# Optimization experiments

Hardware: AMD Instinct MI355X
Metric: run time of the kernel (lower is better)

The kernel has to match this reference:

```python
import jax, jax.numpy as jnp
import numpy as np

IN_F = 4096
OUT_F = 4096
R = 128
E = 8            # expert_num
R_PER = R // E   # per-expert low rank (16)
ALPHA = 16
SCALING = ALPHA / R
N = 8192


def setup_inputs() -> dict:
    key = jax.random.key(0)
    k_x, k_w0, k_g, k_a, k_b = jax.random.split(key, 5)
    x = jax.random.normal(k_x, (N, IN_F), dtype=jnp.float32)
    W0 = jax.random.normal(k_w0, (OUT_F, IN_F), dtype=jnp.float32) * 0.02   # base_layer weight
    Wg = jax.random.normal(k_g, (E, IN_F), dtype=jnp.float32) * 0.02        # GateL weight
    A = jax.random.normal(k_a, (E, R_PER, IN_F), dtype=jnp.float32) * 0.01  # stacked loraA weights
    B = jax.random.normal(k_b, (E, OUT_F, R_PER), dtype=jnp.float32) * 0.01 # stacked loraB weights
    return {"x": x, "W0": W0, "Wg": Wg, "A": A, "B": B}


def reference(x, W0, Wg, A, B):
    # base layer: result = x @ W0^T
    result = jnp.einsum('nd,od->no', x, W0)
    # gate: softmax over experts (dim=1 for 2D input)
    gate = jax.nn.softmax(jnp.einsum('nd,ed->ne', x, Wg), axis=1)  # [N, E]
    # per-expert low-rank: h_i = x @ A_i^T ; y_i = h_i @ B_i^T
    h = jnp.einsum('nd,erd->ner', x, A)        # [N, E, R_PER]
    y = jnp.einsum('ner,eor->neo', h, B)       # [N, E, OUT_F]
    lora = jnp.einsum('neo,ne->no', y, gate)   # gated weighted sum over experts
    return result + SCALING * lora
```

## Files before the change

### kernel.cpp

```cpp
#include <hip/hip_runtime.h>
#include <hip/hip_bf16.h>

#define IN_F   4096
#define OUT_F  4096
#define RTOT   128
#define NE     8
#define RP     16
#define NROWS  8192
#define KC     (IN_F + RTOT)
#define NG     144
#define SCALING 0.125f
#define KSPLIT 4

typedef __attribute__((ext_vector_type(8))) short bf16x8;
typedef __attribute__((ext_vector_type(4))) float f32x4;

__device__ __forceinline__ void gl_lds16(const __hip_bfloat16* g, __hip_bfloat16* l) {
    __builtin_amdgcn_global_load_lds(
        (const __attribute__((address_space(1))) unsigned int*)g,
        (__attribute__((address_space(3))) unsigned int*)l, 16, 0, 0);
}

union bf8pack { bf16x8 v; __hip_bfloat16 h[8]; };
union bf4pack { ushort4 u; __hip_bfloat16 h[4]; };

#define PREP_GRID 33856
__global__ void k_prep(const float* __restrict__ W0, const float* __restrict__ B,
                       const float* __restrict__ A, const float* __restrict__ Wg,
                       const float* __restrict__ x,
                       __hip_bfloat16* __restrict__ Wcat, __hip_bfloat16* __restrict__ AG,
                       __hip_bfloat16* __restrict__ Xcat) {
    int bid = blockIdx.x, tid = threadIdx.x;
    if (bid < 16896) {
        int i4 = (bid * 256 + tid) * 4;
        int o = i4 / KC;
        int c = i4 - o * KC;
        float4 v;
        if (c < IN_F) v = *(const float4*)&W0[(size_t)o * IN_F + c];
        else {
            int k = c - IN_F, e = k >> 4, r = k & 15;
            v = *(const float4*)&B[(size_t)((e * OUT_F + o) << 4) + r];
        }
        bf4pack p;
        p.h[0] = __float2bfloat16(v.x); p.h[1] = __float2bfloat16(v.y);
        p.h[2] = __float2bfloat16(v.z); p.h[3] = __float2bfloat16(v.w);
        *(ushort4*)&Wcat[i4] = p.u;
    } else if (bid < 17472) {
        int j4 = ((bid - 16896) * 256 + tid) * 4;
        int row = j4 >> 12, d = j4 & 4095;
        float4 v = {0.f, 0.f, 0.f, 0.f};
        if (row < RTOT)      v = *(const float4*)&A[j4];
        else if (row < 136)  v = *(const float4*)&Wg[((row - RTOT) << 12) + d];
        bf4pack p;
        p.h[0] = __float2bfloat16(v.x); p.h[1] = __float2bfloat16(v.y);
        p.h[2] = __float2bfloat16(v.z); p.h[3] = __float2bfloat16(v.w);
        *(ushort4*)&AG[j4] = p.u;
    } else {
        int t = (bid - 17472) * 256 + tid;
        int n = t >> 9, c8 = t & 511;
        const float4* src = (const float4*)&x[((size_t)n << 12) + (c8 << 3)];
        float4 v0 = src[0], v1 = src[1];
        bf8pack p;
        p.h[0] = __float2bfloat16(v0.x); p.h[1] = __float2bfloat16(v0.y);
        p.h[2] = __float2bfloat16(v0.z); p.h[3] = __float2bfloat16(v0.w);
        p.h[4] = __float2bfloat16(v1.x); p.h[5] = __float2bfloat16(v1.y);
        p.h[6] = __float2bfloat16(v1.z); p.h[7] = __float2bfloat16(v1.w);
        *(bf16x8*)&Xcat[(size_t)n * KC + (c8 << 3)] = p.v;
    }
}

__global__ __launch_bounds__(256) void k_hgemm(const __hip_bfloat16* __restrict__ Xcat,
                                               const __hip_bfloat16* __restrict__ AG,
                                               float* __restrict__ H) {
    __shared__ __hip_bfloat16 sX[128 * 32];
    __shared__ __hip_bfloat16 sG[NG * 32];
    const int tid  = threadIdx.x;
    const int lane = tid & 63;
    const int w    = tid >> 6;
    const int quad = lane >> 4;
    const int l16  = lane & 15;
    const int m0   = blockIdx.x * 128;
    const int kbeg = blockIdx.y * (IN_F / KSPLIT);

    f32x4 acc[2][9];
    for (int i = 0; i < 2; ++i)
        for (int j = 0; j < 9; ++j)
            acc[i][j] = (f32x4){0.f, 0.f, 0.f, 0.f};

    const int sr = tid >> 2;
    const int sk2 = (((tid & 3) ^ ((sr >> 1) & 3)) << 3);
    const int qq  = quad ^ ((l16 >> 1) & 3);

    for (int kt = kbeg; kt < kbeg + IN_F / KSPLIT; kt += 32) {
        __syncthreads();
        gl_lds16(&Xcat[(size_t)(m0 + sr) * KC + kt + sk2],      &sX[tid * 8]);
        gl_lds16(&Xcat[(size_t)(m0 + 64 + sr) * KC + kt + sk2], &sX[(tid + 256) * 8]);
        gl_lds16(&AG[(size_t)sr * IN_F + kt + sk2],             &sG[tid * 8]);
        gl_lds16(&AG[(size_t)(64 + sr) * IN_F + kt + sk2],      &sG[(tid + 256) * 8]);
        if (tid < 64)
            gl_lds16(&AG[(size_t)(128 + sr) * IN_F + kt + sk2], &sG[(tid + 512) * 8]);
        __syncthreads();

        bf16x8 a[2], b[9];
#pragma unroll
        for (int ti = 0; ti < 2; ++ti)
            a[ti] = *(const bf16x8*)(&sX[(w * 32 + ti * 16 + l16) * 32 + qq * 8]);
#pragma unroll
        for (int tj = 0; tj < 9; ++tj)
            b[tj] = *(const bf16x8*)(&sG[(tj * 16 + l16) * 32 + qq * 8]);
#pragma unroll
        for (int ti = 0; ti < 2; ++ti)
#pragma unroll
            for (int tj = 0; tj < 9; ++tj)
                acc[ti][tj] = __builtin_amdgcn_mfma_f32_16x16x32_bf16(a[ti], b[tj], acc[ti][tj], 0, 0, 0);
    }

    float* Hs = &H[(size_t)blockIdx.y * NROWS * NG];
#pragma unroll
    for (int ti = 0; ti < 2; ++ti)
#pragma unroll
        for (int tj = 0; tj < 9; ++tj) {
            int col = tj * 16 + l16;
#pragma unroll
            for (int i = 0; i < 4; ++i) {
                int row = m0 + w * 32 + ti * 16 + quad * 4 + i;
                Hs[(size_t)row * NG + col] = acc[ti][tj][i];
            }
        }
}

__global__ void k_gate(const float* __restrict__ H, __hip_bfloat16* __restrict__ Xcat) {
    int id = blockIdx.x * 256 + threadIdx.x;
    int n = id >> 4, k8 = id & 15;
    const float* hb = &H[(size_t)n * NG];
    float lg[NE] = {0.f, 0.f, 0.f, 0.f, 0.f, 0.f, 0.f, 0.f};
#pragma unroll
    for (int s = 0; s < KSPLIT; ++s) {
        const float* hs = hb + (size_t)s * NROWS * NG;
        float4 g0 = *(const float4*)&hs[128];
        float4 g1 = *(const float4*)&hs[132];
        lg[0] += g0.x; lg[1] += g0.y; lg[2] += g0.z; lg[3] += g0.w;
        lg[4] += g1.x; lg[5] += g1.y; lg[6] += g1.z; lg[7] += g1.w;
    }
    float mx = lg[0];
#pragma unroll
    for (int e = 1; e < NE; ++e) mx = fmaxf(mx, lg[e]);
    float ssum = 0.f;
#pragma unroll
    for (int e = 0; e < NE; ++e) { lg[e] = __expf(lg[e] - mx); ssum += lg[e]; }
    float inv = SCALING / ssum;
    int e = k8 >> 1;
    float ge = 0.f;
#pragma unroll
    for (int e2 = 0; e2 < NE; ++e2) if (e2 == e) ge = lg[e2];
    ge *= inv;
    float hv[8] = {0.f, 0.f, 0.f, 0.f, 0.f, 0.f, 0.f, 0.f};
#pragma unroll
    for (int s = 0; s < KSPLIT; ++s) {
        const float* hs = hb + (size_t)s * NROWS * NG;
        float4 h0 = *(const float4*)&hs[k8 * 8];
        float4 h1 = *(const float4*)&hs[k8 * 8 + 4];
        hv[0] += h0.x; hv[1] += h0.y; hv[2] += h0.z; hv[3] += h0.w;
        hv[4] += h1.x; hv[5] += h1.y; hv[6] += h1.z; hv[7] += h1.w;
    }
    bf8pack p;
#pragma unroll
    for (int i = 0; i < 8; ++i) p.h[i] = __float2bfloat16(hv[i] * ge);
    *(bf16x8*)&Xcat[(size_t)n * KC + IN_F + k8 * 8] = p.v;
}

__global__ __launch_bounds__(256) void k_gemm(const __hip_bfloat16* __restrict__ Xcat,
                                              const __hip_bfloat16* __restrict__ Wcat,
                                              float* __restrict__ out) {
    __shared__ __hip_bfloat16 sA[128 * 64];
    __shared__ __hip_bfloat16 sB[128 * 64];
    const int tid  = threadIdx.x;
    const int lane = tid & 63;
    const int w    = tid >> 6;
    const int wm   = w >> 1, wn = w & 1;
    const int quad = lane >> 4;
    const int l16  = lane & 15;
    const int m0   = blockIdx.y * 128;
    const int n0   = blockIdx.x * 128;

    f32x4 acc[4][4];
#pragma unroll
    for (int i = 0; i < 4; ++i)
#pragma unroll
        for (int j = 0; j < 4; ++j)
            acc[i][j] = (f32x4){0.f, 0.f, 0.f, 0.f};

    const int srow = tid >> 3;
    const int gc   = (tid & 7) ^ (srow & 7);
    const __hip_bfloat16* gA = &Xcat[(size_t)(m0 + srow) * KC + gc * 8];
    const __hip_bfloat16* gB = &Wcat[(size_t)(n0 + srow) * KC + gc * 8];
    const int xr = l16 & 7;

    for (int kt = 0; kt < KC; kt += 64) {
        __syncthreads();
#pragma unroll
        for (int r = 0; r < 4; ++r) {
            gl_lds16(gA + (size_t)r * 32 * KC + kt, &sA[r * 2048 + tid * 8]);
            gl_lds16(gB + (size_t)r * 32 * KC + kt, &sB[r * 2048 + tid * 8]);
        }
        __syncthreads();

#pragma unroll
        for (int ks = 0; ks < 2; ++ks) {
            bf16x8 a[4], b[4];
#pragma unroll
            for (int t = 0; t < 4; ++t) {
                int ra = wm * 64 + t * 16 + l16;
                int rb = wn * 64 + t * 16 + l16;
                int cofs = ((ks * 4 + quad) ^ xr) * 8;
                a[t] = *(const bf16x8*)(&sA[ra * 64 + cofs]);
                b[t] = *(const bf16x8*)(&sB[rb * 64 + cofs]);
            }
#pragma unroll
            for (int ti = 0; ti < 4; ++ti)
#pragma unroll
                for (int tj = 0; tj < 4; ++tj)
                    acc[ti][tj] = __builtin_amdgcn_mfma_f32_16x16x32_bf16(a[ti], b[tj], acc[ti][tj], 0, 0, 0);
        }
    }

#pragma unroll
    for (int ti = 0; ti < 4; ++ti)
#pragma unroll
        for (int tj = 0; tj < 4; ++tj) {
            int col = n0 + wn * 64 + tj * 16 + l16;
#pragma unroll
            for (int i = 0; i < 4; ++i) {
                int row = m0 + wm * 64 + ti * 16 + quad * 4 + i;
                out[(size_t)row * OUT_F + col] = acc[ti][tj][i];
            }
        }
}

extern "C" void kernel_launch(void* const* d_in, const int* in_sizes, int n_in,
                              void* d_out, int out_size, void* d_ws, size_t ws_size,
                              hipStream_t stream) {
    const float* x  = (const float*)d_in[0];
    const float* W0 = (const float*)d_in[1];
    const float* Wg = (const float*)d_in[2];
    const float* A  = (const float*)d_in[3];
    const float* B  = (const float*)d_in[4];
    float* out = (float*)d_out;

    char* ws = (char*)d_ws;
    size_t off = 0;
    __hip_bfloat16* Xcat = (__hip_bfloat16*)(ws + off); off += (size_t)NROWS * KC * 2;
    __hip_bfloat16* Wcat = (__hip_bfloat16*)(ws + off); off += (size_t)OUT_F * KC * 2;
    __hip_bfloat16* AG   = (__hip_bfloat16*)(ws + off); off += (size_t)NG * IN_F * 2;
    float*          H    = (float*)(ws + off);          off += (size_t)KSPLIT * NROWS * NG * 4;

    k_prep<<<PREP_GRID, 256, 0, stream>>>(W0, B, A, Wg, x, Wcat, AG, Xcat);
    k_hgemm<<<dim3(NROWS / 128, KSPLIT), 256, 0, stream>>>(Xcat, AG, H);
    k_gate<<<(NROWS * 16) / 256, 256, 0, stream>>>(H, Xcat);
    k_gemm<<<dim3(OUT_F / 128, NROWS / 128), 256, 0, stream>>>(Xcat, Wcat, out);
}
```

Before: 563.1 us.

## Rewrite main GEMM as 256x256 tile with double-buffered 8-wave pipelined schedule

The main bf16 GEMM moves from a 128x128 tile with 4 waves and a load/sync/compute loop to a 256x256 tile with 8 waves. Global-to-LDS loads are double-buffered and interleaved with MFMA phases, using explicit barriers, waitcnt and setprio scheduling. Blocks are swizzled for L2 locality. The aim is to hide memory latency and raise reuse, at the cost of 128KB of LDS, heavy register use, and hand-tuned waitcnt logic that is fragile (the tail clamps the K offset and reloads the last tile).

```diff
diff --git a/kernel.cpp b/kernel.cpp
--- a/kernel.cpp
+++ b/kernel.cpp
@@ -169,70 +169,156 @@
     *(bf16x8*)&Xcat[(size_t)n * KC + IN_F + k8 * 8] = p.v;
 }
 
-__global__ __launch_bounds__(256) void k_gemm(const __hip_bfloat16* __restrict__ Xcat,
-                                              const __hip_bfloat16* __restrict__ Wcat,
-                                              float* __restrict__ out) {
-    __shared__ __hip_bfloat16 sA[128 * 64];
-    __shared__ __hip_bfloat16 sB[128 * 64];
+
+#define BARRIER() __builtin_amdgcn_s_barrier()
+#define SBAR()    __builtin_amdgcn_sched_barrier(0)
+#define LGKM0()   do { asm volatile("s_waitcnt lgkmcnt(0)" ::: "memory"); SBAR(); } while (0)
+#define VMCNT6()  asm volatile("s_waitcnt vmcnt(6)" ::: "memory")
+#define VMCNT0()  asm volatile("s_waitcnt vmcnt(0)" ::: "memory")
+#define PRIO(x)   __builtin_amdgcn_s_setprio(x)
+
+#define STAGE(buf, op, half, koff) do {                                               \
+        const __hip_bfloat16* _g = ((op) ? gB : gA) + (size_t)(half) * 128 * KC + (koff); \
+        __hip_bfloat16* _l = lds + ((buf) * 4 + (op) * 2 + (half)) * 8192 + tid * 8;  \
+        gl_lds16(_g, _l);                                                             \
+        gl_lds16(_g + (size_t)64 * KC, _l + 4096);                                    \
+    } while (0)
+
+#define DS_A(b, mbase) do {                                                           \
+        _Pragma("unroll") for (int mi = 0; mi < 4; ++mi) {                            \
+            const __hip_bfloat16* _p = As[b] + (((mbase) + mi) * 16 + l16) * 64;      \
+            a[mi][0] = *(const bf16x8*)(_p + kc0);                                    \
+            a[mi][1] = *(const bf16x8*)(_p + kc1);                                    \
+        } } while (0)
+
+#define DS_B(b, dst, nbase) do {                                                      \
+        _Pragma("unroll") for (int nj = 0; nj < 2; ++nj) {                            \
+            const __hip_bfloat16* _p = Bs[b] + (brow0 + ((nbase) + nj) * 16 + l16) * 64; \
+            dst[nj][0] = *(const bf16x8*)(_p + kc0);                                  \
+            dst[nj][1] = *(const bf16x8*)(_p + kc1);                                  \
+        } } while (0)
+
+#define MM(mb, dst, nb) do {                                                          \
+        _Pragma("unroll") for (int mi = 0; mi < 4; ++mi)                              \
+        _Pragma("unroll") for (int nj = 0; nj < 2; ++nj) {                            \
+            acc[(mb) + mi][(nb) + nj] = __builtin_amdgcn_mfma_f32_16x16x32_bf16(      \
+                a[mi][0], dst[nj][0], acc[(mb) + mi][(nb) + nj], 0, 0, 0);            \
+            acc[(mb) + mi][(nb) + nj] = __builtin_amdgcn_mfma_f32_16x16x32_bf16(      \
+                a[mi][1], dst[nj][1], acc[(mb) + mi][(nb) + nj], 0, 0, 0);            \
+        } } while (0)
+
+__global__ __launch_bounds__(512, 2) void k_gemm(const __hip_bfloat16* __restrict__ Xcat,
+                                                 const __hip_bfloat16* __restrict__ Wcat,
+                                                 float* __restrict__ out) {
+    __shared__ __hip_bfloat16 lds[8 * 8192];
     const int tid  = threadIdx.x;
     const int lane = tid & 63;
     const int w    = tid >> 6;
-    const int wm   = w >> 1, wn = w & 1;
+    const int wm   = w >> 2, wn = w & 3;
     const int quad = lane >> 4;
     const int l16  = lane & 15;
-    const int m0   = blockIdx.y * 128;
-    const int n0   = blockIdx.x * 128;
-
-    f32x4 acc[4][4];
-#pragma unroll
-    for (int i = 0; i < 4; ++i)
+    const int xr   = l16 & 7;
+
+    const int bid = blockIdx.x;
+    const int swz = (bid & 7) * 64 + (bid >> 3);
+    const int m0  = (swz >> 4) * 256;
+    const int n0  = (swz & 15) * 256;
+
+    const int srow = tid >> 3;
+    const int scol = ((tid & 7) ^ (srow & 7)) << 3;
+    const __hip_bfloat16* gA = Xcat + (size_t)(m0 + srow) * KC + scol;
+    const __hip_bfloat16* gB = Wcat + (size_t)(n0 + srow) * KC + scol;
+
+    const __hip_bfloat16* As[2] = { lds + (0 + wm) * 8192,        lds + (4 + wm) * 8192 };
+    const __hip_bfloat16* Bs[2] = { lds + (2 + (wn >> 1)) * 8192, lds + (6 + (wn >> 1)) * 8192 };
+    const int brow0 = (wn & 1) * 64;
+    const int kc0 = (quad ^ xr) * 8;
+    const int kc1 = ((4 + quad) ^ xr) * 8;
+
+    f32x4 acc[8][4];
+#pragma unroll
+    for (int i = 0; i < 8; ++i)
 #pragma unroll
         for (int j = 0; j < 4; ++j)
             acc[i][j] = (f32x4){0.f, 0.f, 0.f, 0.f};
-
-    const int srow = tid >> 3;
-    const int gc   = (tid & 7) ^ (srow & 7);
-    const __hip_bfloat16* gA = &Xcat[(size_t)(m0 + srow) * KC + gc * 8];
-    const __hip_bfloat16* gB = &Wcat[(size_t)(n0 + srow) * KC + gc * 8];
-    const int xr = l16 & 7;
-
-    for (int kt = 0; kt < KC; kt += 64) {
-        __syncthreads();
-#pragma unroll
-        for (int r = 0; r < 4; ++r) {
-            gl_lds16(gA + (size_t)r * 32 * KC + kt, &sA[r * 2048 + tid * 8]);
-            gl_lds16(gB + (size_t)r * 32 * KC + kt, &sB[r * 2048 + tid * 8]);
-        }
-        __syncthreads();
-
-#pragma unroll
-        for (int ks = 0; ks < 2; ++ks) {
-            bf16x8 a[4], b[4];
-#pragma unroll
-            for (int t = 0; t < 4; ++t) {
-                int ra = wm * 64 + t * 16 + l16;
-                int rb = wn * 64 + t * 16 + l16;
-                int cofs = ((ks * 4 + quad) ^ xr) * 8;
-                a[t] = *(const bf16x8*)(&sA[ra * 64 + cofs]);
-                b[t] = *(const bf16x8*)(&sB[rb * 64 + cofs]);
-            }
-#pragma unroll
-            for (int ti = 0; ti < 4; ++ti)
-#pragma unroll
-                for (int tj = 0; tj < 4; ++tj)
-                    acc[ti][tj] = __builtin_amdgcn_mfma_f32_16x16x32_bf16(a[ti], b[tj], acc[ti][tj], 0, 0, 0);
-        }
-    }
-
-#pragma unroll
-    for (int ti = 0; ti < 4; ++ti)
+    bf16x8 a[4][2], bl[2][2], bh[2][2];
+
+    STAGE(0, 1, 0, 0);
+    STAGE(0, 1, 1, 0);
+    STAGE(0, 0, 0, 0);
+    STAGE(0, 0, 1, 0);
+    STAGE(1, 1, 0, 64);
+    STAGE(1, 1, 1, 64);
+    STAGE(1, 0, 0, 64);
+    VMCNT6();
+    BARRIER(); SBAR();
+
+#pragma unroll 1
+    for (int i = 0; i < 33; ++i) {
+        const int kb    = i * 128;
+        const int t1off = kb + 64;
+        const int s0off = (kb + 128 <= KC - 64) ? kb + 128 : KC - 64;
+        const int s1off = (kb + 192 <= KC - 64) ? kb + 192 : KC - 64;
+
+        DS_A(0, 0); DS_B(0, bl, 0);
+        STAGE(1, 0, 1, t1off);
+        BARRIER(); LGKM0();
+        PRIO(1); MM(0, bl, 0); PRIO(0);
+        BARRIER(); SBAR();
+
+        DS_B(0, bh, 2);
+        BARRIER(); LGKM0();
+        PRIO(1); MM(0, bh, 2); PRIO(0);
+        BARRIER(); SBAR();
+
+        DS_A(0, 4);
+        STAGE(0, 1, 0, s0off);
+        STAGE(0, 1, 1, s0off);
+        BARRIER(); LGKM0();
+        PRIO(1); MM(4, bh, 2); PRIO(0);
+        BARRIER(); SBAR();
+
+        STAGE(0, 0, 0, s0off);
+        BARRIER(); LGKM0();
+        PRIO(1); MM(4, bl, 0); PRIO(0);
+        VMCNT6();
+        BARRIER(); SBAR();
+
+        DS_A(1, 0); DS_B(1, bl, 0);
+        STAGE(0, 0, 1, s0off);
+        BARRIER(); LGKM0();
+        PRIO(1); MM(0, bl, 0); PRIO(0);
+        BARRIER(); SBAR();
+
+        DS_B(1, bh, 2);
+        BARRIER(); LGKM0();
+        PRIO(1); MM(0, bh, 2); PRIO(0);
+        BARRIER(); SBAR();
+
+        DS_A(1, 4);
+        STAGE(1, 1, 0, s1off);
+        STAGE(1, 1, 1, s1off);
+        BARRIER(); LGKM0();
+        PRIO(1); MM(4, bh, 2); PRIO(0);
+        BARRIER(); SBAR();
+
+        STAGE(1, 0, 0, s1off);
+        BARRIER(); LGKM0();
+        PRIO(1); MM(4, bl, 0); PRIO(0);
+        VMCNT6();
+        BARRIER(); SBAR();
+    }
+    VMCNT0();
+
+#pragma unroll
+    for (int ti = 0; ti < 8; ++ti)
 #pragma unroll
         for (int tj = 0; tj < 4; ++tj) {
             int col = n0 + wn * 64 + tj * 16 + l16;
 #pragma unroll
-            for (int i = 0; i < 4; ++i) {
-                int row = m0 + wm * 64 + ti * 16 + quad * 4 + i;
-                out[(size_t)row * OUT_F + col] = acc[ti][tj][i];
+            for (int r = 0; r < 4; ++r) {
+                int row = m0 + wm * 128 + ti * 16 + quad * 4 + r;
+                out[(size_t)row * OUT_F + col] = acc[ti][tj][r];
             }
         }
 }
@@ -257,5 +343,5 @@
     k_prep<<<PREP_GRID, 256, 0, stream>>>(W0, B, A, Wg, x, Wcat, AG, Xcat);
     k_hgemm<<<dim3(NROWS / 128, KSPLIT), 256, 0, stream>>>(Xcat, AG, H);
     k_gate<<<(NROWS * 16) / 256, 256, 0, stream>>>(H, Xcat);
-    k_gemm<<<dim3(OUT_F / 128, NROWS / 128), 256, 0, stream>>>(Xcat, Wcat, out);
-}
+    k_gemm<<<512, 512, 0, stream>>>(Xcat, Wcat, out);
+}
```

Result: faster. 522.1 us (-7.3%).
